# Performance work log

Hardware: AMD Instinct MI355X
Metric: run time of the kernel (lower is better)

The kernel has to match this reference:

```python
import jax, jax.numpy as jnp
import numpy as np

# Static conv / spline hyperparameters (match init_kwargs)
KH = KW = 3
SH = SW = 1          # stride
DH = DW = 1          # dilation
GRID_SIZE = 5
SPLINE_ORDER = 3
N_CONVS = 8


def _extract_patches(x):
    """im2col unfold. x: (B,C,H,W) -> (B,C,Ho,Wo,KH*KW), valid padding."""
    B, C, H, W = x.shape
    Ho = (H - (KH - 1) * DH - 1) // SH + 1
    Wo = (W - (KW - 1) * DW - 1) // SW + 1
    cols = []
    for i in range(KH):
        for j in range(KW):
            cols.append(x[:, :,
                          i * DH: i * DH + (Ho - 1) * SH + 1: SH,
                          j * DW: j * DW + (Wo - 1) * SW + 1: SW])
    return jnp.stack(cols, axis=-1), Ho, Wo


def _b_splines(xf, grid):
    """Cox-de Boor recursion. xf: (P,K), grid: (K, G+2*so+1) -> (P,K,G+so)."""
    x = xf[:, :, None]
    bases = ((x >= grid[:, :-1]) & (x < grid[:, 1:])).astype(xf.dtype)
    for k in range(1, SPLINE_ORDER + 1):
        bases = ((x - grid[:, :-(k + 1)]) / (grid[:, k:-1] - grid[:, :-(k + 1)])
                 * bases[:, :, :-1]
                 + (grid[:, k + 1:] - x) / (grid[:, k + 1:] - grid[:, 1:-k])
                 * bases[:, :, 1:])
    return bases


def setup_inputs() -> dict:
    key = jax.random.key(0)
    k0, k1, k2, k3 = jax.random.split(key, 4)
    B, C, H, W = 8, 32, 64, 64
    K = KH * KW                       # in_features of KANLinear = 9
    coeff = GRID_SIZE + SPLINE_ORDER  # spline coefficients per input = 8
    # activations inside grid_range [-1, 1]
    x = jax.random.uniform(k0, (B, C, H, W), jnp.float32, -1.0, 1.0)
    # grid buffer: arange(-so, gs+so+1)*h + grid_range[0], tiled per input feature
    h = (1.0 - (-1.0)) / GRID_SIZE
    g = jnp.arange(-SPLINE_ORDER, GRID_SIZE + SPLINE_ORDER + 1,
                   dtype=jnp.float32) * h - 1.0
    grid = jnp.tile(g[None, :], (K, 1))  # (K, 12)
    base_weight = jax.random.normal(k1, (N_CONVS, K), jnp.float32) / np.sqrt(K)
    spline_weight = jax.random.normal(k2, (N_CONVS, K, coeff), jnp.float32) * 0.1
    spline_scaler = jax.random.normal(k3, (N_CONVS, K), jnp.float32) / np.sqrt(K) + 1.0
    return {"x": x, "grid": grid, "base_weight": base_weight,
            "spline_weight": spline_weight, "spline_scaler": spline_scaler}


def reference(x, grid, base_weight, spline_weight, spline_scaler):
    B, C, H, W = x.shape
    patches, Ho, Wo = _extract_patches(x)          # (B,C,Ho,Wo,K)
    K = KH * KW
    xf = patches.reshape(-1, K)                    # (P, K), P = B*C*Ho*Wo
    # KANLinear: base path (SiLU + linear) + spline path (B-spline basis + linear)
    base_out = jnp.einsum('pk,vk->pv', jax.nn.silu(xf), base_weight)
    bases = _b_splines(xf, grid)                   # (P, K, coeff)
    scaled_sw = spline_weight * spline_scaler[:, :, None]
    spline_out = jnp.einsum('pkc,vkc->pv', bases, scaled_sw)
    out = (base_out + spline_out).reshape(B, C, Ho, Wo, N_CONVS)
    # channel-major then conv ordering: out[:, kern + channel*n_convs]
    return out.transpose(0, 1, 4, 2, 3).reshape(B, C * N_CONVS, Ho, Wo)
```

## Files before the change

kernel.cpp:

```cpp
#include <hip/hip_runtime.h>

#define NV 8
#define HO 62
#define WO 62

__global__ __launch_bounds__(256, 4) void kan_conv_sparse(
    const float* __restrict__ x,
    const float* __restrict__ grid,
    const float* __restrict__ bw,
    const float* __restrict__ sw,
    const float* __restrict__ sc,
    float* __restrict__ out)
{
    __shared__ float wspl[4][5][9][4];

    const int tid  = threadIdx.x;
    const int lane = tid & 63;
    const int vl   = tid >> 6;

    const int item  = blockIdx.x;
    const int plane = item >> 4;
    const int chunk = (item >> 1) & 7;
    const int half  = item & 1;
    const int v     = half * 4 + vl;

    for (int i = tid; i < 720; i += 256) {
        const int m  = i & 3;
        const int kk = (i >> 2) % 9;
        const int jj = (i / 36) % 5;
        const int wl = i / 180;
        const int wv = half * 4 + wl;
        wspl[wl][jj][kk][m] = sw[(wv * 9 + kk) * 8 + jj + m] * sc[wv * 9 + kk];
    }

    float wb[9];
    #pragma unroll
    for (int kk = 0; kk < 9; ++kk) wb[kk] = bw[v * 9 + kk];

    const float g0    = grid[0];
    const float inv_h = 1.0f / (grid[1] - grid[0]);

    __syncthreads();

    const int r0 = chunk * 8;
    const float* xp = x + (size_t)plane * 4096;
    float* op = out + (size_t)(plane * NV + v) * (HO * WO);

    float acc[3] = {0.0f, 0.0f, 0.0f};

    #pragma unroll
    for (int k = 0; k < 10; ++k) {
        const int rr  = r0 + k;
        const int row = (rr < 64) ? rr : 63;
        const float xv = xp[row * 64 + lane];

        const float s = xv / (1.0f + __expf(-xv));
        const float u = (xv - g0) * inv_h;
        int j = (int)floorf(u);
        j = (j < 3) ? 3 : ((j > 7) ? 7 : j);
        const float t   = u - (float)j;
        const float omt = 1.0f - t;
        const float t2  = t * t;
        const float t3  = t2 * t;
        const float c6  = 1.0f / 6.0f;
        const float bA  = omt * omt * omt * c6;
        const float bB  = (3.0f * t3 - 6.0f * t2 + 4.0f) * c6;
        const float bC  = (-3.0f * t3 + 3.0f * t2 + 3.0f * t + 1.0f) * c6;
        const float bD  = t3 * c6;

        float D[9];
        #pragma unroll
        for (int kk = 0; kk < 9; ++kk) {
            const float4 w4 = *reinterpret_cast<const float4*>(&wspl[vl][j - 3][kk][0]);
            D[kk] = fmaf(s, wb[kk],
                     fmaf(bA, w4.x, fmaf(bB, w4.y, fmaf(bC, w4.z, bD * w4.w))));
        }

        const float d01 = __shfl(D[1], lane + 1, 64);
        const float d02 = __shfl(D[2], lane + 2, 64);
        const float d11 = __shfl(D[4], lane + 1, 64);
        const float d12 = __shfl(D[5], lane + 2, 64);
        const float d21 = __shfl(D[7], lane + 1, 64);
        const float d22 = __shfl(D[8], lane + 2, 64);

        acc[k % 3] = D[0] + d01 + d02;
        if (k >= 1) acc[(k + 2) % 3] += D[3] + d11 + d12;
        if (k >= 2) {
            acc[(k + 1) % 3] += D[6] + d21 + d22;
            const int ho = rr - 2;
            if (ho < HO && lane < WO)
                op[ho * WO + lane] = acc[(k + 1) % 3];
        }
    }
}

extern "C" void kernel_launch(void* const* d_in, const int* in_sizes, int n_in,
                              void* d_out, int out_size, void* d_ws, size_t ws_size,
                              hipStream_t stream) {
    const float* x    = (const float*)d_in[0];
    const float* grid = (const float*)d_in[1];
    const float* bw   = (const float*)d_in[2];
    const float* sw   = (const float*)d_in[3];
    const float* sc   = (const float*)d_in[4];
    float* out = (float*)d_out;

    kan_conv_sparse<<<4096, 256, 0, stream>>>(x, grid, bw, sw, sc, out);
}
```

Before: 96.15 us.

## Recast KAN conv as fp16 MFMA GEMM over sparse spline features in LDS

```diff
diff --git a/kernel.cpp b/kernel.cpp
--- a/kernel.cpp
+++ b/kernel.cpp
@@ -1,10 +1,13 @@
 #include <hip/hip_runtime.h>
 
-#define NV 8
+typedef _Float16 f16;
+typedef _Float16 f16x8 __attribute__((ext_vector_type(8)));
+typedef float    f32x4 __attribute__((ext_vector_type(4)));
+
 #define HO 62
 #define WO 62
 
-__global__ __launch_bounds__(256, 4) void kan_conv_sparse(
+__global__ __launch_bounds__(512, 4) void kan_conv_mfma(
     const float* __restrict__ x,
     const float* __restrict__ grid,
     const float* __restrict__ bw,
@@ -12,47 +15,50 @@
     const float* __restrict__ sc,
     float* __restrict__ out)
 {
-    __shared__ float wspl[4][5][9][4];
+    __shared__ __align__(16) f16 feat[19456];
 
     const int tid  = threadIdx.x;
     const int lane = tid & 63;
-    const int vl   = tid >> 6;
+    const int w    = tid >> 6;
 
-    const int item  = blockIdx.x;
-    const int plane = item >> 4;
-    const int chunk = (item >> 1) & 7;
-    const int half  = item & 1;
-    const int v     = half * 4 + vl;
+    const int bx    = blockIdx.x;
+    const int plane = bx >> 2;
+    const int chunk = bx & 3;
+    const int r0    = (chunk < 3) ? chunk * 16 : 46;
 
-    for (int i = tid; i < 720; i += 256) {
-        const int m  = i & 3;
-        const int kk = (i >> 2) % 9;
-        const int jj = (i / 36) % 5;
-        const int wl = i / 180;
-        const int wv = half * 4 + wl;
-        wspl[wl][jj][kk][m] = sw[(wv * 9 + kk) * 8 + jj + m] * sc[wv * 9 + kk];
+    const int nn = lane & 15;
+    const int kb = lane >> 4;
+    f16x8 bfrag[3][2];
+    #pragma unroll
+    for (int ki = 0; ki < 3; ++ki) {
+        #pragma unroll
+        for (int kjp = 0; kjp < 2; ++kjp) {
+            f16x8 bf;
+            #pragma unroll
+            for (int e = 0; e < 8; ++e) {
+                const int k    = kb * 8 + e;
+                const int kj   = kjp * 2 + (k >> 4);
+                const int slot = k & 15;
+                float wv = 0.0f;
+                if (nn < 8 && kj < 3 && slot < 9) {
+                    const int kk = ki * 3 + kj;
+                    wv = (slot == 0) ? bw[nn * 9 + kk]
+                                     : sw[(nn * 9 + kk) * 8 + (slot - 1)] * sc[nn * 9 + kk];
+                }
+                bf[e] = (f16)wv;
+            }
+            bfrag[ki][kjp] = bf;
+        }
     }
-
-    float wb[9];
-    #pragma unroll
-    for (int kk = 0; kk < 9; ++kk) wb[kk] = bw[v * 9 + kk];
 
     const float g0    = grid[0];
     const float inv_h = 1.0f / (grid[1] - grid[0]);
+    const float* xp   = x + (size_t)plane * 4096;
 
-    __syncthreads();
-
-    const int r0 = chunk * 8;
-    const float* xp = x + (size_t)plane * 4096;
-    float* op = out + (size_t)(plane * NV + v) * (HO * WO);
-
-    float acc[3] = {0.0f, 0.0f, 0.0f};
-
-    #pragma unroll
-    for (int k = 0; k < 10; ++k) {
-        const int rr  = r0 + k;
-        const int row = (rr < 64) ? rr : 63;
-        const float xv = xp[row * 64 + lane];
+    for (int idx = tid; idx < 18 * 64; idx += 512) {
+        const int row = idx >> 6;
+        const int col = idx & 63;
+        const float xv = xp[(r0 + row) * 64 + col];
 
         const float s = xv / (1.0f + __expf(-xv));
         const float u = (xv - g0) * inv_h;
@@ -63,33 +69,63 @@
         const float t2  = t * t;
         const float t3  = t2 * t;
         const float c6  = 1.0f / 6.0f;
-        const float bA  = omt * omt * omt * c6;
-        const float bB  = (3.0f * t3 - 6.0f * t2 + 4.0f) * c6;
-        const float bC  = (-3.0f * t3 + 3.0f * t2 + 3.0f * t + 1.0f) * c6;
-        const float bD  = t3 * c6;
+        float bv[4];
+        bv[0] = omt * omt * omt * c6;
+        bv[1] = (3.0f * t3 - 6.0f * t2 + 4.0f) * c6;
+        bv[2] = (-3.0f * t3 + 3.0f * t2 + 3.0f * t + 1.0f) * c6;
+        bv[3] = t3 * c6;
 
-        float D[9];
+        const int base0 = row * 1024 + col * 8;
+        f16x8 z0 = {(f16)s, (f16)0.f, (f16)0.f, (f16)0.f,
+                    (f16)0.f, (f16)0.f, (f16)0.f, (f16)0.f};
+        f16x8 z1 = {(f16)0.f, (f16)0.f, (f16)0.f, (f16)0.f,
+                    (f16)0.f, (f16)0.f, (f16)0.f, (f16)0.f};
+        *(f16x8*)&feat[base0]       = z0;
+        *(f16x8*)&feat[base0 + 512] = z1;
         #pragma unroll
-        for (int kk = 0; kk < 9; ++kk) {
-            const float4 w4 = *reinterpret_cast<const float4*>(&wspl[vl][j - 3][kk][0]);
-            D[kk] = fmaf(s, wb[kk],
-                     fmaf(bA, w4.x, fmaf(bB, w4.y, fmaf(bC, w4.z, bD * w4.w))));
+        for (int m = 0; m < 4; ++m) {
+            const int slot = j - 2 + m;
+            feat[row * 1024 + (slot >> 3) * 512 + col * 8 + (slot & 7)] = (f16)bv[m];
         }
+    }
+    for (int idx = tid; idx < 128; idx += 512) {
+        f16x8 z = {(f16)0.f, (f16)0.f, (f16)0.f, (f16)0.f,
+                   (f16)0.f, (f16)0.f, (f16)0.f, (f16)0.f};
+        *(f16x8*)&feat[18432 + idx * 8] = z;
+    }
+    __syncthreads();
 
-        const float d01 = __shfl(D[1], lane + 1, 64);
-        const float d02 = __shfl(D[2], lane + 2, 64);
-        const float d11 = __shfl(D[4], lane + 1, 64);
-        const float d12 = __shfl(D[5], lane + 2, 64);
-        const float d21 = __shfl(D[7], lane + 1, 64);
-        const float d22 = __shfl(D[8], lane + 2, 64);
+    const int mI    = lane & 15;
+    const int khalf = kb & 1;
+    const int cAdd  = kb >> 1;
 
-        acc[k % 3] = D[0] + d01 + d02;
-        if (k >= 1) acc[(k + 2) % 3] += D[3] + d11 + d12;
-        if (k >= 2) {
-            acc[(k + 1) % 3] += D[6] + d21 + d22;
-            const int ho = rr - 2;
-            if (ho < HO && lane < WO)
-                op[ho * WO + lane] = acc[(k + 1) % 3];
+    for (int u = w; u < 64; u += 8) {
+        const int ro = u >> 2;
+        const int c0 = (u & 3) * 16;
+        f32x4 acc = {0.f, 0.f, 0.f, 0.f};
+        #pragma unroll
+        for (int ki = 0; ki < 3; ++ki) {
+            #pragma unroll
+            for (int kjp = 0; kjp < 2; ++kjp) {
+                const int col = c0 + mI + kjp * 2 + cAdd;
+                const f16x8 a = *(const f16x8*)&feat[(ro + ki) * 1024 + khalf * 512 + col * 8];
+                acc = __builtin_amdgcn_mfma_f32_16x16x32_f16(a, bfrag[ki][kjp], acc, 0, 0, 0);
+            }
+        }
+        if (nn < 8) {
+            const int rowg = r0 + ro;
+            const int colb = c0 + kb * 4;
+            float* po = out + ((size_t)(plane * 8 + nn) * (HO * WO)) + rowg * WO + colb;
+            if (c0 < 48) {
+                float2 lo = {acc[0], acc[1]};
+                float2 hi = {acc[2], acc[3]};
+                *(float2*)po       = lo;
+                *(float2*)(po + 2) = hi;
+            } else {
+                #pragma unroll
+                for (int i = 0; i < 4; ++i)
+                    if (colb + i < WO) po[i] = acc[i];
+            }
         }
     }
 }
@@ -104,5 +140,5 @@
     const float* sc   = (const float*)d_in[4];
     float* out = (float*)d_out;
 
-    kan_conv_sparse<<<4096, 256, 0, stream>>>(x, grid, bw, sw, sc, out);
+    kan_conv_mfma<<<1024, 512, 0, stream>>>(x, grid, bw, sw, sc, out);
 }
```

Result: faster. 94.18 us (-2.0%).
